# Optimization experiments

Hardware: AMD Instinct MI355X
Metric: run time of the kernel (lower is better)

Reference implementation:

```python
import jax, jax.numpy as jnp
import numpy as np

N_SUB = 60000   # nodes in current subgraph (rows of fnode/agraph/subnode)
M = 120000      # total messages (directed edges)
K = 8           # max neighbors per node/message
H = 128         # hidden_size
IN = 256        # input_size (fmess feature dim)
FD = 128        # node_fdim
DEPTH = 2       # rnn depth (sparse_forward iterations)
NUM_NODES = 65536


def setup_inputs() -> dict:
    key = jax.random.key(0)
    ks = jax.random.split(key, 12)
    s = 0.05
    def w(k, shape):
        return jax.random.normal(k, shape, jnp.float32) * s
    return {
        "fnode": jax.random.normal(ks[0], (N_SUB, FD), jnp.float32),
        "fmess": jax.random.normal(ks[1], (M, IN), jnp.float32),
        "agraph": jax.random.randint(ks[2], (N_SUB, K), 0, M, dtype=jnp.int32),
        "bgraph": jax.random.randint(ks[3], (M, K), 0, M, dtype=jnp.int32),
        "h_in": jax.random.normal(ks[4], (M, H), jnp.float32),
        "c_in": jax.random.normal(ks[5], (M, H), jnp.float32),
        "submess": jnp.arange(N_SUB, dtype=jnp.int32),
        "subnode": jnp.arange(N_SUB, dtype=jnp.int32),
        "num_nodes": NUM_NODES,
        # tree-LSTM gate weights, stored [in_dim, out_dim]
        "Wi": w(ks[6], (IN + H, H)), "bi": jnp.zeros((H,), jnp.float32),
        "Wo": w(ks[7], (IN + H, H)), "bo": jnp.zeros((H,), jnp.float32),
        "Wf": w(ks[8], (IN + H, H)), "bf": jnp.zeros((H,), jnp.float32),
        "Wu": w(ks[9], (IN + H, H)), "bu": jnp.zeros((H,), jnp.float32),
        # node readout W_o: Linear(node_fdim + hidden -> hidden) + ReLU (+ Dropout = eval no-op)
        "Wn": w(ks[10], (FD + H, H)), "bn": jnp.zeros((H,), jnp.float32),
    }


def _lstm_cell(x, h_nei, c_nei, Wi, bi, Wo, bo, Wf, bf, Wu, bu):
    # x: [S, IN]; h_nei, c_nei: [S, K, H]  (hgraph-style child-sum tree LSTM)
    h_sum = h_nei.sum(axis=1)                         # [S, H]
    z = jnp.concatenate([x, h_sum], axis=-1)          # [S, IN+H]
    i = jax.nn.sigmoid(z @ Wi + bi)
    o = jax.nn.sigmoid(z @ Wo + bo)
    u = jnp.tanh(z @ Wu + bu)
    # per-neighbor forget gate: sigmoid(cat([x_expand, h_nei]) @ Wf + bf),
    # split the matmul so we never materialize the [S, K, IN+H] concat
    d_in = x.shape[1]
    fx = x @ Wf[:d_in] + bf                           # [S, H]
    f = jax.nn.sigmoid(fx[:, None, :] + h_nei @ Wf[d_in:])  # [S, K, H]
    c = i * u + (f * c_nei).sum(axis=1)
    h = o * jnp.tanh(c)
    return h, c


def reference(fnode, fmess, agraph, bgraph, h_in, c_in, submess, subnode, num_nodes,
              Wi, bi, Wo, bo, Wf, bf, Wu, bu, Wn, bn):
    # LSTM.sparse_forward: zero state at submess rows, then iteratively update them
    mask = jnp.ones((h_in.shape[0],), h_in.dtype).at[submess].set(0.0)
    h = h_in * mask[:, None]
    c = c_in * mask[:, None]
    x_sub = fmess[submess]       # [S, IN]
    bg_sub = bgraph[submess]     # [S, K] message-neighbor ids
    for _ in range(DEPTH):
        h_nei = h[bg_sub]        # [S, K, H] gather
        c_nei = c[bg_sub]
        sub_h, sub_c = _lstm_cell(x_sub, h_nei, c_nei, Wi, bi, Wo, bo, Wf, bf, Wu, bu)
        h = h.at[submess].set(sub_h)   # index_scatter
        c = c.at[submess].set(sub_c)
    # node update: gather incoming messages, sum, Linear + ReLU (dropout inactive at eval)
    nei_message = h[agraph].sum(axis=1)                      # [N_SUB, H]
    node_hiddens = jnp.concatenate([fnode, nei_message], axis=-1)
    node_hiddens = jax.nn.relu(node_hiddens @ Wn + bn)       # [N_SUB, H]
    node_buf = jnp.zeros((num_nodes, node_hiddens.shape[1]), node_hiddens.dtype)
    node_buf = node_buf.at[subnode].set(node_hiddens)        # index_scatter into full buffer
    return node_buf, h, c
```

## Files before the change

### kernel.cpp

```cpp
#include <hip/hip_runtime.h>
#include <cstdint>
#include <cstddef>

#define Hc   128
#define INc  256
#define Kc   8
#define HP   136
#define HSP  136
#define EPH  136
#define ZP2  264
#define XOP  520

typedef unsigned short ushortT;
typedef __attribute__((ext_vector_type(8))) short bf16x8;
typedef __attribute__((ext_vector_type(4))) float f32x4;
typedef __attribute__((ext_vector_type(4))) unsigned short us4;
typedef __attribute__((ext_vector_type(8))) unsigned short us8;

__device__ __forceinline__ float fsig(float x) {
  return __builtin_amdgcn_rcpf(1.f + __expf(-x));
}
__device__ __forceinline__ float ftanh(float x) {
  float e = __expf(2.f * fminf(x, 15.f));
  return (e - 1.f) * __builtin_amdgcn_rcpf(e + 1.f);
}
__device__ __forceinline__ ushortT f2bf(float f) {
  unsigned u = __builtin_bit_cast(unsigned, f);
  unsigned r = (u + 0x7fffu + ((u >> 16) & 1u)) >> 16;
  return (ushortT)r;
}
__device__ __forceinline__ us4 f2bf4(float4 v) {
  us4 o; o[0] = f2bf(v.x); o[1] = f2bf(v.y); o[2] = f2bf(v.z); o[3] = f2bf(v.w);
  return o;
}
__device__ __forceinline__ us8 f2bf8(float4 a, float4 b) {
  us8 o;
  o[0] = f2bf(a.x); o[1] = f2bf(a.y); o[2] = f2bf(a.z); o[3] = f2bf(a.w);
  o[4] = f2bf(b.x); o[5] = f2bf(b.y); o[6] = f2bf(b.z); o[7] = f2bf(b.w);
  return o;
}
__device__ __forceinline__ float bf2f(ushortT u) {
  return __builtin_bit_cast(float, (unsigned)u << 16);
}

#define GATE_FRAGS (4*8*12*64)
#define WN_FRAGS   (8*8*64)

__global__ void marks_init(int* __restrict__ mark, int M, int* __restrict__ nmark, int NN) {
  int i = blockIdx.x * blockDim.x + threadIdx.x;
  if (i < M) mark[i] = -1;
  if (i < NN) nmark[i] = -1;
}

__global__ void set_repack(const int* __restrict__ submess, const int* __restrict__ subnode,
                           int S, int* __restrict__ mark, int* __restrict__ nmark,
                           const float* __restrict__ Wi, const float* __restrict__ Wo,
                           const float* __restrict__ Wu, const float* __restrict__ Wf,
                           const float* __restrict__ Wn, ushortT* __restrict__ pack, int SB) {
  if ((int)blockIdx.x < SB) {
    int i = blockIdx.x * 256 + threadIdx.x;
    if (i < S) { mark[submess[i]] = i; nmark[subnode[i]] = i; }
    return;
  }
  int idx = (blockIdx.x - SB) * 256 + threadIdx.x;
  if (idx < GATE_FRAGS) {
    int lane = idx & 63;
    int kt = (idx >> 6) % 12;
    int gc = idx / (64 * 12);
    int c = gc & 7, g = gc >> 3;
    const float* W = (g == 0) ? Wi : (g == 1) ? Wo : (g == 2) ? Wu : Wf;
    int k0 = kt * 32 + (lane >> 4) * 8;
    int col = c * 16 + (lane & 15);
    ushortT* dst = pack + (size_t)idx * 8;
    #pragma unroll
    for (int j = 0; j < 8; ++j) dst[j] = f2bf(W[(size_t)(k0 + j) * Hc + col]);
  } else if (idx < GATE_FRAGS + WN_FRAGS) {
    int i2 = idx - GATE_FRAGS;
    int lane = i2 & 63;
    int kt = (i2 >> 6) & 7;
    int c = i2 >> 9;
    int k0 = kt * 32 + (lane >> 4) * 8;
    int col = c * 16 + (lane & 15);
    ushortT* dst = pack + (size_t)GATE_FRAGS * 8 + (size_t)i2 * 8;
    #pragma unroll
    for (int j = 0; j < 8; ++j) dst[j] = f2bf(Wn[(size_t)(k0 + j) * Hc + col]);
  }
}

__device__ __forceinline__ const bf16x8* wh_frag(const ushortT* pack, int g, int cw, int kf, int lane) {
  return (const bf16x8*)&pack[(size_t)(((g * 8 + cw) * 12 + (8 + kf)) * 64 + lane) * 8];
}

__global__ __launch_bounds__(256) void xg_stage_hf(
    const float* __restrict__ fmess, const int* __restrict__ submess,
    const ushortT* __restrict__ pack,
    const float* __restrict__ bi, const float* __restrict__ bo,
    const float* __restrict__ bu, const float* __restrict__ bfb,
    ushortT* __restrict__ Xg,
    const float* __restrict__ h_in, const float* __restrict__ c_in,
    const int* __restrict__ mark,
    float* __restrict__ h_out, float* __restrict__ c_out,
    ushortT* __restrict__ H16x, ushortT* __restrict__ C16x, ushortT* __restrict__ Hf16x,
    int M, int S, int XB)
{
  __shared__ __align__(16) unsigned char pool[16 * XOP * 2];
  __shared__ int aux[16];
  const int t = threadIdx.x;
  const int w = t >> 6, lane = t & 63, lg = lane >> 4, cl = lane & 15;

  if ((int)blockIdx.x < XB) {
    ushortT* xs = (ushortT*)pool;
    ushortT* xo = (ushortT*)pool;
    const int row0 = blockIdx.x * 16;
    if (t < 16) aux[t] = (row0 + t < S) ? submess[row0 + t] : -1;
    __syncthreads();
    {
      int r = t >> 4, cp = t & 15;
      int ms = aux[r];
      const float4* xr = (ms >= 0) ? (const float4*)(fmess + (size_t)ms * INc) : nullptr;
      #pragma unroll
      for (int q = 0; q < 4; ++q) {
        int slot = cp + q * 16;
        float4 v;
        if (xr) v = xr[slot]; else { v.x = v.y = v.z = v.w = 0.f; }
        *(us4*)&xs[r * ZP2 + slot * 4] = f2bf4(v);
      }
    }
    __syncthreads();

    f32x4 acc[8];
    #pragma unroll
    for (int i = 0; i < 8; ++i) acc[i] = (f32x4){0.f, 0.f, 0.f, 0.f};
    const ushortT* zr = &xs[cl * ZP2 + lg * 8];
    #pragma unroll
    for (int kt = 0; kt < 8; ++kt) {
      bf16x8 a = *(const bf16x8*)&zr[kt * 32];
      #pragma unroll
      for (int c = 0; c < 8; ++c) {
        bf16x8 b = *(const bf16x8*)&pack[(size_t)(((w * 8 + c) * 12 + kt) * 64 + lane) * 8];
        acc[c] = __builtin_amdgcn_mfma_f32_16x16x32_bf16(a, b, acc[c], 0, 0, 0);
      }
    }
    __syncthreads();
    const float* bias = (w == 0) ? bi : (w == 1) ? bo : (w == 2) ? bu : bfb;
    #pragma unroll
    for (int c = 0; c < 8; ++c) {
      int col = c * 16 + cl;
      float bv = bias[col];
      #pragma unroll
      for (int reg = 0; reg < 4; ++reg)
        xo[(lg * 4 + reg) * XOP + w * 128 + col] = f2bf(acc[c][reg] + bv);
    }
    __syncthreads();
    {
      int r = t >> 4, cc = t & 15;
      int s = row0 + r;
      if (s < S) {
        const ushortT* src = &xo[r * XOP + cc * 32];
        ushortT* dst = &Xg[(size_t)s * 512 + cc * 32];
        *(us8*)&dst[0]  = *(const us8*)&src[0];
        *(us8*)&dst[8]  = *(const us8*)&src[8];
        *(us8*)&dst[16] = *(const us8*)&src[16];
        *(us8*)&dst[24] = *(const us8*)&src[24];
      }
    }
    return;
  }

  ushortT* zh = (ushortT*)pool;
  int* mk = aux;
  const int row0 = (blockIdx.x - XB) * 16;

  if (blockIdx.x == XB && t < 48) {
    int arr = t >> 4, cp = t & 15;
    ushortT* dst = (arr == 0) ? H16x : (arr == 1) ? C16x : Hf16x;
    us8 z;
    #pragma unroll
    for (int e = 0; e < 8; ++e) z[e] = 0;
    *(us8*)&dst[(size_t)(M + S) * Hc + cp * 8] = z;
  }
  if (t < 16) mk[t] = (row0 + t < M) ? mark[row0 + t] : 0;
  __syncthreads();
  {
    int r = t >> 4, cp = t & 15;
    int j = row0 + r;
    us8 hz;
    #pragma unroll
    for (int e = 0; e < 8; ++e) hz[e] = 0;
    if (j < M && mk[r] < 0) {
      const float4* h4 = (const float4*)(h_in + (size_t)j * Hc);
      const float4* c4 = (const float4*)(c_in + (size_t)j * Hc);
      float4 a0 = h4[cp * 2], a1 = h4[cp * 2 + 1];
      float4 b0 = c4[cp * 2], b1 = c4[cp * 2 + 1];
      ((float4*)(h_out + (size_t)j * Hc))[cp * 2] = a0;
      ((float4*)(h_out + (size_t)j * Hc))[cp * 2 + 1] = a1;
      ((float4*)(c_out + (size_t)j * Hc))[cp * 2] = b0;
      ((float4*)(c_out + (size_t)j * Hc))[cp * 2 + 1] = b1;
      us8 h8 = f2bf8(a0, a1);
      *(us8*)&H16x[(size_t)j * Hc + cp * 8] = h8;
      *(us8*)&C16x[(size_t)j * Hc + cp * 8] = f2bf8(b0, b1);
      hz = h8;
    }
    *(us8*)&zh[r * HP + cp * 8] = hz;
  }
  __syncthreads();

  f32x4 acc0 = (f32x4){0.f,0.f,0.f,0.f}, acc1 = acc0;
  const ushortT* zr = &zh[cl * HP + lg * 8];
  #pragma unroll
  for (int kf = 0; kf < 4; ++kf) {
    bf16x8 a = *(const bf16x8*)&zr[kf * 32];
    acc0 = __builtin_amdgcn_mfma_f32_16x16x32_bf16(a, *wh_frag(pack, 3, w*2+0, kf, lane), acc0, 0, 0, 0);
    acc1 = __builtin_amdgcn_mfma_f32_16x16x32_bf16(a, *wh_frag(pack, 3, w*2+1, kf, lane), acc1, 0, 0, 0);
  }
  __syncthreads();
  #pragma unroll
  for (int half = 0; half < 2; ++half) {
    int col = (w * 2 + half) * 16 + cl;
    f32x4 a_ = half ? acc1 : acc0;
    #pragma unroll
    for (int reg = 0; reg < 4; ++reg)
      zh[(lg * 4 + reg) * HP + col] = f2bf(a_[reg]);
  }
  __syncthreads();
  {
    int r = t >> 4, cp = t & 15;
    if (row0 + r < M && mk[r] < 0)
      *(us8*)&Hf16x[(size_t)(row0 + r) * Hc + cp * 8] = *(const us8*)&zh[r * HP + cp * 8];
  }
}

template<int MODE>
__global__ __launch_bounds__(256) void lstm8(
    const int* __restrict__ submess, const int* __restrict__ bgraph,
    const int* __restrict__ mark,
    ushortT* H16x, ushortT* C16x, ushortT* Hf16x,
    const ushortT* __restrict__ Xg, const ushortT* __restrict__ pack,
    ushortT* hsumNS, ushortT* cpartNS,
    float* __restrict__ dstH, float* __restrict__ dstC, int S, int M)
{
  __shared__ __align__(16) ushortT zs[16 * HSP];
  __shared__ __align__(16) ushortT pih[16 * EPH];
  __shared__ __align__(16) ushortT poh[16 * EPH];
  __shared__ __align__(16) ushortT puh[16 * EPH];
  __shared__ int nbj[16][Kc];
  __shared__ int msrow[16];

  const int t = threadIdx.x;
  const int row0 = blockIdx.x * 16;
  const int DUMMY = M + S;

  if (t < 128) {
    int r = t >> 3, k = t & 7;
    int s = row0 + r;
    int ms = (s < S) ? submess[s] : -1;
    if (k == 0) msrow[r] = ms;
    int j = DUMMY;
    if (ms >= 0) {
      int jj = bgraph[(size_t)ms * Kc + k];
      int m = mark[jj];
      j = (MODE == 0) ? (m >= 0 ? DUMMY : jj) : (m >= 0 ? M + m : DUMMY);
    }
    nbj[r][k] = j;
  }
  __syncthreads();

  {
    int r = t >> 4, cp = t & 15;
    int spos = row0 + r;
    float sum[8] = {0.f,0.f,0.f,0.f,0.f,0.f,0.f,0.f};
    if (MODE == 1 && spos < S) {
      us8 hs = *(const us8*)&hsumNS[(size_t)spos * Hc + cp * 8];
      #pragma unroll
      for (int e = 0; e < 8; ++e) sum[e] = bf2f(hs[e]);
    }
    #pragma unroll
    for (int k = 0; k < Kc; ++k) {
      int j = nbj[r][k];
      us8 v = *(const us8*)&H16x[(size_t)j * Hc + cp * 8];
      #pragma unroll
      for (int e = 0; e < 8; ++e) sum[e] += bf2f(v[e]);
    }
    us8 o8;
    #pragma unroll
    for (int e = 0; e < 8; ++e) o8[e] = f2bf(sum[e]);
    *(us8*)&zs[r * HSP + cp * 8] = o8;
    if (MODE == 0 && spos < S)
      *(us8*)&hsumNS[(size_t)spos * Hc + cp * 8] = o8;
  }
  __syncthreads();

  const int w = t >> 6, lane = t & 63, lg = lane >> 4, cl = lane & 15;

  f32x4 acc[6];
  #pragma unroll
  for (int i = 0; i < 6; ++i) acc[i] = (f32x4){0.f, 0.f, 0.f, 0.f};
  const ushortT* zrow = &zs[cl * HSP + lg * 8];
  #pragma unroll
  for (int kf = 0; kf < 4; ++kf) {
    bf16x8 a = *(const bf16x8*)&zrow[kf * 32];
    #pragma unroll
    for (int g = 0; g < 3; ++g)
      #pragma unroll
      for (int half = 0; half < 2; ++half)
        acc[g * 2 + half] = __builtin_amdgcn_mfma_f32_16x16x32_bf16(
            a, *wh_frag(pack, g, w * 2 + half, kf, lane), acc[g * 2 + half], 0, 0, 0);
  }

  #pragma unroll
  for (int half = 0; half < 2; ++half) {
    int col = (w * 2 + half) * 16 + cl;
    #pragma unroll
    for (int reg = 0; reg < 4; ++reg) {
      int row = lg * 4 + reg;
      pih[row * EPH + col] = f2bf(acc[0 + half][reg]);
      poh[row * EPH + col] = f2bf(acc[2 + half][reg]);
      puh[row * EPH + col] = f2bf(acc[4 + half][reg]);
    }
  }
  __syncthreads();

  {
    int r = t >> 4, cc = t & 15;
    int ms = msrow[r];
    int spos = row0 + r;
    const ushortT* xgr = Xg + (size_t)spos * 512 + cc * 8;
    us8 xi8 = *(const us8*)&xgr[0];
    us8 xo8 = *(const us8*)&xgr[128];
    us8 xu8 = *(const us8*)&xgr[256];
    us8 xf8 = *(const us8*)&xgr[384];
    us8 pi8 = *(const us8*)&pih[r * EPH + cc * 8];
    us8 po8 = *(const us8*)&poh[r * EPH + cc * 8];
    us8 pu8 = *(const us8*)&puh[r * EPH + cc * 8];
    float fx[8], ovv[8], iu[8], cn[8];
    #pragma unroll
    for (int e = 0; e < 8; ++e) {
      float iv = fsig(bf2f(xi8[e]) + bf2f(pi8[e]));
      float uv = ftanh(bf2f(xu8[e]) + bf2f(pu8[e]));
      ovv[e] = fsig(bf2f(xo8[e]) + bf2f(po8[e]));
      fx[e] = bf2f(xf8[e]);
      iu[e] = iv * uv;
      cn[e] = 0.f;
    }
    #pragma unroll
    for (int k = 0; k < Kc; ++k) {
      int j = nbj[r][k];
      us8 hf8 = *(const us8*)&Hf16x[(size_t)j * Hc + cc * 8];
      us8 cn8 = *(const us8*)&C16x[(size_t)j * Hc + cc * 8];
      #pragma unroll
      for (int e = 0; e < 8; ++e)
        cn[e] = fmaf(fsig(fx[e] + bf2f(hf8[e])), bf2f(cn8[e]), cn[e]);
    }
    float cacc[8];
    if (MODE == 1 && spos < S) {
      us8 cp8 = *(const us8*)&cpartNS[(size_t)spos * Hc + cc * 8];
      #pragma unroll
      for (int e = 0; e < 8; ++e) cacc[e] = iu[e] + cn[e] + bf2f(cp8[e]);
    } else {
      #pragma unroll
      for (int e = 0; e < 8; ++e) cacc[e] = iu[e] + cn[e];
    }
    float hv[8];
    #pragma unroll
    for (int e = 0; e < 8; ++e) hv[e] = ovv[e] * ftanh(cacc[e]);

    if (MODE == 0) {
      us8 h8, c8, cn16;
      #pragma unroll
      for (int e = 0; e < 8; ++e) {
        h8[e] = (spos < S) ? f2bf(hv[e]) : (ushortT)0;
        c8[e] = f2bf(cacc[e]);
        cn16[e] = f2bf(cn[e]);
      }
      if (spos < S) {
        *(us8*)&H16x[(size_t)(M + spos) * Hc + cc * 8] = h8;
        *(us8*)&C16x[(size_t)(M + spos) * Hc + cc * 8] = c8;
        *(us8*)&cpartNS[(size_t)spos * Hc + cc * 8] = cn16;
      }
      *(us8*)&zs[r * HSP + cc * 8] = h8;
    } else {
      if (ms >= 0) {
        float* dh = dstH + (size_t)ms * Hc + cc * 8;
        float* dc = dstC + (size_t)ms * Hc + cc * 8;
        *(float4*)&dh[0] = *(float4*)&hv[0];
        *(float4*)&dh[4] = *(float4*)&hv[4];
        *(float4*)&dc[0] = *(float4*)&cacc[0];
        *(float4*)&dc[4] = *(float4*)&cacc[4];
      }
    }
  }

  if (MODE == 0) {
    __syncthreads();
    f32x4 a0 = (f32x4){0.f,0.f,0.f,0.f}, a1 = a0;
    const ushortT* zr2 = &zs[cl * HSP + lg * 8];
    #pragma unroll
    for (int kf = 0; kf < 4; ++kf) {
      bf16x8 a = *(const bf16x8*)&zr2[kf * 32];
      a0 = __builtin_amdgcn_mfma_f32_16x16x32_bf16(a, *wh_frag(pack, 3, w*2+0, kf, lane), a0, 0, 0, 0);
      a1 = __builtin_amdgcn_mfma_f32_16x16x32_bf16(a, *wh_frag(pack, 3, w*2+1, kf, lane), a1, 0, 0, 0);
    }
    #pragma unroll
    for (int half = 0; half < 2; ++half) {
      int col = (w * 2 + half) * 16 + cl;
      f32x4 a_ = half ? a1 : a0;
      #pragma unroll
      for (int reg = 0; reg < 4; ++reg)
        pih[(lg * 4 + reg) * EPH + col] = f2bf(a_[reg]);
    }
    __syncthreads();
    {
      int r = t >> 4, cp = t & 15;
      int sp = row0 + r;
      if (sp < S)
        *(us8*)&Hf16x[(size_t)(M + sp) * Hc + cp * 8] = *(const us8*)&pih[r * EPH + cp * 8];
    }
  }
}

__global__ __launch_bounds__(256) void readout_zero(
    const float* __restrict__ fnode, const int* __restrict__ agraph,
    const int* __restrict__ subnode, const float* __restrict__ h_out,
    const ushortT* __restrict__ H16x, const int* __restrict__ mark,
    const int* __restrict__ nmark,
    const ushortT* __restrict__ packWn, const float* __restrict__ bn,
    float* __restrict__ node_buf, int Nsub, int num_nodes, int NB, int ZB)
{
  __shared__ __align__(16) ushortT z2[16 * ZP2];
  __shared__ int orow[16];
  __shared__ int jn[16][Kc];

  const int t = threadIdx.x;

  if ((int)blockIdx.x >= NB) {
    long total = (long)num_nodes * 16;
    float4 z; z.x = z.y = z.z = z.w = 0.f;
    for (long idx = (long)(blockIdx.x - NB) * 256 + t; idx < total; idx += (long)ZB * 256) {
      long v = idx >> 4;
      int cp = (int)(idx & 15);
      if (nmark[v] < 0) {
        ((float4*)(node_buf + (size_t)v * Hc))[cp * 2] = z;
        ((float4*)(node_buf + (size_t)v * Hc))[cp * 2 + 1] = z;
      }
    }
    return;
  }

  const int row0 = blockIdx.x * 16;
  if (t < 16) orow[t] = (row0 + t < Nsub) ? subnode[row0 + t] : -1;
  if (t >= 64 && t < 64 + 128) {
    int i = t - 64, r = i >> 3, k = i & 7;
    int v = row0 + r;
    int j = 0;
    if (v < Nsub) {
      j = agraph[(size_t)v * Kc + k];
      if (mark[j] >= 0) j = ~j;
    }
    jn[r][k] = j;
  }
  {
    int r = t >> 4, cp = t & 15;
    int v = row0 + r;
    const float4* fr = (v < Nsub) ? (const float4*)(fnode + (size_t)v * Hc) : nullptr;
    float4 v0, v1; v0.x = v0.y = v0.z = v0.w = 0.f; v1 = v0;
    if (fr) { v0 = fr[cp]; v1 = fr[cp + 16]; }
    *(us4*)&z2[r * ZP2 + cp * 4] = f2bf4(v0);
    *(us4*)&z2[r * ZP2 + 64 + cp * 4] = f2bf4(v1);
  }
  __syncthreads();
  {
    int r = t >> 4, cp = t & 15;
    float sum[8] = {0.f,0.f,0.f,0.f,0.f,0.f,0.f,0.f};
    #pragma unroll
    for (int k = 0; k < Kc; ++k) {
      int je = jn[r][k];
      if (je < 0) {
        int j = ~je;
        float4 p0 = ((const float4*)(h_out + (size_t)j * Hc))[cp * 2];
        float4 p1 = ((const float4*)(h_out + (size_t)j * Hc))[cp * 2 + 1];
        sum[0] += p0.x; sum[1] += p0.y; sum[2] += p0.z; sum[3] += p0.w;
        sum[4] += p1.x; sum[5] += p1.y; sum[6] += p1.z; sum[7] += p1.w;
      } else {
        us8 v = *(const us8*)&H16x[(size_t)je * Hc + cp * 8];
        #pragma unroll
        for (int e = 0; e < 8; ++e) sum[e] += bf2f(v[e]);
      }
    }
    us8 o8;
    #pragma unroll
    for (int e = 0; e < 8; ++e) o8[e] = f2bf(sum[e]);
    *(us8*)&z2[r * ZP2 + Hc + cp * 8] = o8;
  }
  __syncthreads();

  const int w = t >> 6, lane = t & 63;
  const int lg = lane >> 4, cl = lane & 15;

  f32x4 acc0 = (f32x4){0.f,0.f,0.f,0.f};
  f32x4 acc1 = (f32x4){0.f,0.f,0.f,0.f};
  const ushortT* zr = &z2[cl * ZP2 + lg * 8];
  #pragma unroll
  for (int kt = 0; kt < 8; ++kt) {
    bf16x8 a = *(const bf16x8*)&zr[kt * 32];
    bf16x8 b0 = *(const bf16x8*)&packWn[(size_t)(((w * 2 + 0) * 8 + kt) * 64 + lane) * 8];
    bf16x8 b1 = *(const bf16x8*)&packWn[(size_t)(((w * 2 + 1) * 8 + kt) * 64 + lane) * 8];
    acc0 = __builtin_amdgcn_mfma_f32_16x16x32_bf16(a, b0, acc0, 0, 0, 0);
    acc1 = __builtin_amdgcn_mfma_f32_16x16x32_bf16(a, b1, acc1, 0, 0, 0);
  }
  __syncthreads();
  float* zf = (float*)z2;
  #pragma unroll
  for (int half = 0; half < 2; ++half) {
    int col = (w * 2 + half) * 16 + cl;
    float bnv = bn[col];
    f32x4 a_ = half ? acc1 : acc0;
    #pragma unroll
    for (int reg = 0; reg < 4; ++reg)
      zf[(lg * 4 + reg) * 132 + col] = fmaxf(a_[reg] + bnv, 0.f);
  }
  __syncthreads();
  {
    int r = t >> 4, cc = t & 15;
    int o = orow[r];
    if (o >= 0) {
      float* dst = node_buf + (size_t)o * Hc + cc * 8;
      *(float4*)&dst[0] = *(const float4*)&zf[r * 132 + cc * 8];
      *(float4*)&dst[4] = *(const float4*)&zf[r * 132 + cc * 8 + 4];
    }
  }
}

extern "C" void kernel_launch(void* const* d_in, const int* in_sizes, int n_in,
                              void* d_out, int out_size, void* d_ws, size_t ws_size,
                              hipStream_t stream) {
  const float* fnode   = (const float*)d_in[0];
  const float* fmess   = (const float*)d_in[1];
  const int*   agraph  = (const int*)d_in[2];
  const int*   bgraph  = (const int*)d_in[3];
  const float* h_in    = (const float*)d_in[4];
  const float* c_in    = (const float*)d_in[5];
  const int*   submess = (const int*)d_in[6];
  const int*   subnode = (const int*)d_in[7];
  const float* Wi = (const float*)d_in[9];
  const float* bi = (const float*)d_in[10];
  const float* Wo = (const float*)d_in[11];
  const float* bo = (const float*)d_in[12];
  const float* Wf = (const float*)d_in[13];
  const float* bf_ = (const float*)d_in[14];
  const float* Wu = (const float*)d_in[15];
  const float* bu = (const float*)d_in[16];
  const float* Wn = (const float*)d_in[17];
  const float* bn = (const float*)d_in[18];

  const int S    = in_sizes[6];
  const int Nsub = in_sizes[2] / Kc;
  const int M    = in_sizes[4] / Hc;
  const int num_nodes = out_size / Hc - 2 * M;

  float* node_buf = (float*)d_out;
  float* h_out = node_buf + (size_t)num_nodes * Hc;
  float* c_out = h_out + (size_t)M * Hc;

  const int lblocks = (S + 15) / 16;

  int* mark = (int*)d_ws;
  size_t off = (((size_t)M * sizeof(int)) + 255) & ~(size_t)255;
  int* nmark = (int*)((char*)d_ws + off);
  off += (((size_t)num_nodes * sizeof(int)) + 255) & ~(size_t)255;
  ushortT* pack = (ushortT*)((char*)d_ws + off);
  off += (((size_t)(GATE_FRAGS + WN_FRAGS) * 8 * sizeof(ushortT)) + 255) & ~(size_t)255;
  size_t shadow_bytes = (((size_t)(M + S + 1) * Hc * sizeof(ushortT)) + 255) & ~(size_t)255;
  ushortT* Hf16x = (ushortT*)((char*)d_ws + off); off += shadow_bytes;
  ushortT* C16x  = (ushortT*)((char*)d_ws + off); off += shadow_bytes;
  ushortT* H16x  = (ushortT*)((char*)d_ws + off); off += shadow_bytes;
  ushortT* Xg    = (ushortT*)((char*)d_ws + off);
  ushortT* packWn = pack + (size_t)GATE_FRAGS * 8;
  ushortT* cpartNS = (ushortT*)node_buf;
  ushortT* hsumNS  = cpartNS + (size_t)S * Hc;

  int initN = (M > num_nodes) ? M : num_nodes;
  hipLaunchKernelGGL(marks_init, dim3((initN + 255) / 256), dim3(256), 0, stream,
                     mark, M, nmark, num_nodes);
  {
    int SB = (S + 255) / 256;
    int RB = (GATE_FRAGS + WN_FRAGS + 255) / 256;
    hipLaunchKernelGGL(set_repack, dim3(SB + RB), dim3(256), 0, stream,
                       submess, subnode, S, mark, nmark, Wi, Wo, Wu, Wf, Wn, pack, SB);
  }
  {
    int XB = lblocks;
    int SB2 = (M + 15) / 16;
    hipLaunchKernelGGL(xg_stage_hf, dim3(XB + SB2), dim3(256), 0, stream,
                       fmess, submess, pack, bi, bo, bu, bf_, Xg,
                       h_in, c_in, mark, h_out, c_out, H16x, C16x, Hf16x,
                       M, S, XB);
  }
  hipLaunchKernelGGL(lstm8<0>, dim3(lblocks), dim3(256), 0, stream,
      submess, bgraph, mark, H16x, C16x, Hf16x, Xg, pack,
      hsumNS, cpartNS, h_out, c_out, S, M);
  hipLaunchKernelGGL(lstm8<1>, dim3(lblocks), dim3(256), 0, stream,
      submess, bgraph, mark, H16x, C16x, Hf16x, Xg, pack,
      hsumNS, cpartNS, h_out, c_out, S, M);
  {
    int NB = (Nsub + 15) / 16;
    int ZB = 512;
    hipLaunchKernelGGL(readout_zero, dim3(NB + ZB), dim3(256), 0, stream,
        fnode, agraph, subnode, h_out, H16x, mark, nmark, packWn, bn,
        node_buf, Nsub, num_nodes, NB, ZB);
  }
}
```

Baseline: 278.6 us.

## Interleave H/C/Hf bf16 shadows into one row array and double rows per Xg block

Merges the three separate bf16 shadow arrays (H, C, forget-gate H projection) into one interleaved array with a 384-element row stride, so a neighbor gather of c and hf for the same message hits adjacent memory in one row. Separately, the Xg precompute blocks now handle 32 rows instead of 16, reusing each loaded weight fragment for two MFMA row tiles. The first targets scattered gather traffic across three buffers; the second halves weight fragment reloads in the input projection at the cost of more accumulator registers and fewer blocks. The H-only gathers now stride over larger rows, which may reduce cache-line density for those reads.

```diff
diff --git a/kernel.cpp b/kernel.cpp
--- a/kernel.cpp
+++ b/kernel.cpp
@@ -10,6 +10,7 @@
 #define EPH  136
 #define ZP2  264
 #define XOP  520
+#define HCS  384
 
 typedef unsigned short ushortT;
 typedef __attribute__((ext_vector_type(8))) short bf16x8;
@@ -100,22 +101,21 @@
     const float* __restrict__ h_in, const float* __restrict__ c_in,
     const int* __restrict__ mark,
     float* __restrict__ h_out, float* __restrict__ c_out,
-    ushortT* __restrict__ H16x, ushortT* __restrict__ C16x, ushortT* __restrict__ Hf16x,
+    ushortT* __restrict__ HCF,
     int M, int S, int XB)
 {
-  __shared__ __align__(16) unsigned char pool[16 * XOP * 2];
-  __shared__ int aux[16];
+  __shared__ __align__(16) ushortT xs[32 * ZP2];
+  __shared__ int aux[32];
   const int t = threadIdx.x;
   const int w = t >> 6, lane = t & 63, lg = lane >> 4, cl = lane & 15;
 
   if ((int)blockIdx.x < XB) {
-    ushortT* xs = (ushortT*)pool;
-    ushortT* xo = (ushortT*)pool;
-    const int row0 = blockIdx.x * 16;
-    if (t < 16) aux[t] = (row0 + t < S) ? submess[row0 + t] : -1;
+    const int row0 = blockIdx.x * 32;
+    if (t < 32) aux[t] = (row0 + t < S) ? submess[row0 + t] : -1;
     __syncthreads();
-    {
-      int r = t >> 4, cp = t & 15;
+    #pragma unroll
+    for (int rr = 0; rr < 2; ++rr) {
+      int r = (t >> 4) + rr * 16, cp = t & 15;
       int ms = aux[r];
       const float4* xr = (ms >= 0) ? (const float4*)(fmess + (size_t)ms * INc) : nullptr;
       #pragma unroll
@@ -128,56 +128,66 @@
     }
     __syncthreads();
 
-    f32x4 acc[8];
-    #pragma unroll
-    for (int i = 0; i < 8; ++i) acc[i] = (f32x4){0.f, 0.f, 0.f, 0.f};
-    const ushortT* zr = &xs[cl * ZP2 + lg * 8];
+    f32x4 acc0[8], acc1[8];
+    #pragma unroll
+    for (int i = 0; i < 8; ++i) {
+      acc0[i] = (f32x4){0.f, 0.f, 0.f, 0.f};
+      acc1[i] = (f32x4){0.f, 0.f, 0.f, 0.f};
+    }
+    const ushortT* zrA = &xs[cl * ZP2 + lg * 8];
+    const ushortT* zrB = &xs[(16 + cl) * ZP2 + lg * 8];
     #pragma unroll
     for (int kt = 0; kt < 8; ++kt) {
-      bf16x8 a = *(const bf16x8*)&zr[kt * 32];
+      bf16x8 a0 = *(const bf16x8*)&zrA[kt * 32];
+      bf16x8 a1 = *(const bf16x8*)&zrB[kt * 32];
       #pragma unroll
       for (int c = 0; c < 8; ++c) {
         bf16x8 b = *(const bf16x8*)&pack[(size_t)(((w * 8 + c) * 12 + kt) * 64 + lane) * 8];
-        acc[c] = __builtin_amdgcn_mfma_f32_16x16x32_bf16(a, b, acc[c], 0, 0, 0);
+        acc0[c] = __builtin_amdgcn_mfma_f32_16x16x32_bf16(a0, b, acc0[c], 0, 0, 0);
+        acc1[c] = __builtin_amdgcn_mfma_f32_16x16x32_bf16(a1, b, acc1[c], 0, 0, 0);
       }
     }
     __syncthreads();
     const float* bias = (w == 0) ? bi : (w == 1) ? bo : (w == 2) ? bu : bfb;
     #pragma unroll
-    for (int c = 0; c < 8; ++c) {
-      int col = c * 16 + cl;
-      float bv = bias[col];
-      #pragma unroll
-      for (int reg = 0; reg < 4; ++reg)
-        xo[(lg * 4 + reg) * XOP + w * 128 + col] = f2bf(acc[c][reg] + bv);
-    }
-    __syncthreads();
-    {
-      int r = t >> 4, cc = t & 15;
-      int s = row0 + r;
-      if (s < S) {
-        const ushortT* src = &xo[r * XOP + cc * 32];
-        ushortT* dst = &Xg[(size_t)s * 512 + cc * 32];
-        *(us8*)&dst[0]  = *(const us8*)&src[0];
-        *(us8*)&dst[8]  = *(const us8*)&src[8];
-        *(us8*)&dst[16] = *(const us8*)&src[16];
-        *(us8*)&dst[24] = *(const us8*)&src[24];
-      }
+    for (int mt = 0; mt < 2; ++mt) {
+      #pragma unroll
+      for (int c = 0; c < 8; ++c) {
+        int col = c * 16 + cl;
+        float bv = bias[col];
+        #pragma unroll
+        for (int reg = 0; reg < 4; ++reg) {
+          float v = (mt ? acc1[c][reg] : acc0[c][reg]) + bv;
+          xs[(lg * 4 + reg) * XOP + w * 128 + col] = f2bf(v);
+        }
+      }
+      __syncthreads();
+      {
+        int r = t >> 4, cc = t & 15;
+        int s = row0 + mt * 16 + r;
+        if (s < S) {
+          const ushortT* src = &xs[r * XOP + cc * 32];
+          ushortT* dst = &Xg[(size_t)s * 512 + cc * 32];
+          *(us8*)&dst[0]  = *(const us8*)&src[0];
+          *(us8*)&dst[8]  = *(const us8*)&src[8];
+          *(us8*)&dst[16] = *(const us8*)&src[16];
+          *(us8*)&dst[24] = *(const us8*)&src[24];
+        }
+      }
+      __syncthreads();
     }
     return;
   }
 
-  ushortT* zh = (ushortT*)pool;
+  ushortT* zh = xs;
   int* mk = aux;
   const int row0 = (blockIdx.x - XB) * 16;
 
   if (blockIdx.x == XB && t < 48) {
-    int arr = t >> 4, cp = t & 15;
-    ushortT* dst = (arr == 0) ? H16x : (arr == 1) ? C16x : Hf16x;
     us8 z;
     #pragma unroll
     for (int e = 0; e < 8; ++e) z[e] = 0;
-    *(us8*)&dst[(size_t)(M + S) * Hc + cp * 8] = z;
+    *(us8*)&HCF[(size_t)(M + S) * HCS + t * 8] = z;
   }
   if (t < 16) mk[t] = (row0 + t < M) ? mark[row0 + t] : 0;
   __syncthreads();
@@ -197,8 +207,8 @@
       ((float4*)(c_out + (size_t)j * Hc))[cp * 2] = b0;
       ((float4*)(c_out + (size_t)j * Hc))[cp * 2 + 1] = b1;
       us8 h8 = f2bf8(a0, a1);
-      *(us8*)&H16x[(size_t)j * Hc + cp * 8] = h8;
-      *(us8*)&C16x[(size_t)j * Hc + cp * 8] = f2bf8(b0, b1);
+      *(us8*)&HCF[(size_t)j * HCS + cp * 8] = h8;
+      *(us8*)&HCF[(size_t)j * HCS + 128 + cp * 8] = f2bf8(b0, b1);
       hz = h8;
     }
     *(us8*)&zh[r * HP + cp * 8] = hz;
@@ -226,7 +236,7 @@
   {
     int r = t >> 4, cp = t & 15;
     if (row0 + r < M && mk[r] < 0)
-      *(us8*)&Hf16x[(size_t)(row0 + r) * Hc + cp * 8] = *(const us8*)&zh[r * HP + cp * 8];
+      *(us8*)&HCF[(size_t)(row0 + r) * HCS + 256 + cp * 8] = *(const us8*)&zh[r * HP + cp * 8];
   }
 }
 
@@ -234,7 +244,7 @@
 __global__ __launch_bounds__(256) void lstm8(
     const int* __restrict__ submess, const int* __restrict__ bgraph,
     const int* __restrict__ mark,
-    ushortT* H16x, ushortT* C16x, ushortT* Hf16x,
+    ushortT* HCF,
     const ushortT* __restrict__ Xg, const ushortT* __restrict__ pack,
     ushortT* hsumNS, ushortT* cpartNS,
     float* __restrict__ dstH, float* __restrict__ dstC, int S, int M)
@@ -277,7 +287,7 @@
     #pragma unroll
     for (int k = 0; k < Kc; ++k) {
       int j = nbj[r][k];
-      us8 v = *(const us8*)&H16x[(size_t)j * Hc + cp * 8];
+      us8 v = *(const us8*)&HCF[(size_t)j * HCS + cp * 8];
       #pragma unroll
       for (int e = 0; e < 8; ++e) sum[e] += bf2f(v[e]);
     }
@@ -345,8 +355,8 @@
     #pragma unroll
     for (int k = 0; k < Kc; ++k) {
       int j = nbj[r][k];
-      us8 hf8 = *(const us8*)&Hf16x[(size_t)j * Hc + cc * 8];
-      us8 cn8 = *(const us8*)&C16x[(size_t)j * Hc + cc * 8];
+      us8 hf8 = *(const us8*)&HCF[(size_t)j * HCS + 256 + cc * 8];
+      us8 cn8 = *(const us8*)&HCF[(size_t)j * HCS + 128 + cc * 8];
       #pragma unroll
       for (int e = 0; e < 8; ++e)
         cn[e] = fmaf(fsig(fx[e] + bf2f(hf8[e])), bf2f(cn8[e]), cn[e]);
@@ -373,8 +383,8 @@
         cn16[e] = f2bf(cn[e]);
       }
       if (spos < S) {
-        *(us8*)&H16x[(size_t)(M + spos) * Hc + cc * 8] = h8;
-        *(us8*)&C16x[(size_t)(M + spos) * Hc + cc * 8] = c8;
+        *(us8*)&HCF[(size_t)(M + spos) * HCS + cc * 8] = h8;
+        *(us8*)&HCF[(size_t)(M + spos) * HCS + 128 + cc * 8] = c8;
         *(us8*)&cpartNS[(size_t)spos * Hc + cc * 8] = cn16;
       }
       *(us8*)&zs[r * HSP + cc * 8] = h8;
@@ -413,7 +423,7 @@
       int r = t >> 4, cp = t & 15;
       int sp = row0 + r;
       if (sp < S)
-        *(us8*)&Hf16x[(size_t)(M + sp) * Hc + cp * 8] = *(const us8*)&pih[r * EPH + cp * 8];
+        *(us8*)&HCF[(size_t)(M + sp) * HCS + 256 + cp * 8] = *(const us8*)&pih[r * EPH + cp * 8];
     }
   }
 }
@@ -421,7 +431,7 @@
 __global__ __launch_bounds__(256) void readout_zero(
     const float* __restrict__ fnode, const int* __restrict__ agraph,
     const int* __restrict__ subnode, const float* __restrict__ h_out,
-    const ushortT* __restrict__ H16x, const int* __restrict__ mark,
+    const ushortT* __restrict__ HCF, const int* __restrict__ mark,
     const int* __restrict__ nmark,
     const ushortT* __restrict__ packWn, const float* __restrict__ bn,
     float* __restrict__ node_buf, int Nsub, int num_nodes, int NB, int ZB)
@@ -481,7 +491,7 @@
         sum[0] += p0.x; sum[1] += p0.y; sum[2] += p0.z; sum[3] += p0.w;
         sum[4] += p1.x; sum[5] += p1.y; sum[6] += p1.z; sum[7] += p1.w;
       } else {
-        us8 v = *(const us8*)&H16x[(size_t)je * Hc + cp * 8];
+        us8 v = *(const us8*)&HCF[(size_t)je * HCS + cp * 8];
         #pragma unroll
         for (int e = 0; e < 8; ++e) sum[e] += bf2f(v[e]);
       }
@@ -569,11 +579,9 @@
   off += (((size_t)num_nodes * sizeof(int)) + 255) & ~(size_t)255;
   ushortT* pack = (ushortT*)((char*)d_ws + off);
   off += (((size_t)(GATE_FRAGS + WN_FRAGS) * 8 * sizeof(ushortT)) + 255) & ~(size_t)255;
-  size_t shadow_bytes = (((size_t)(M + S + 1) * Hc * sizeof(ushortT)) + 255) & ~(size_t)255;
-  ushortT* Hf16x = (ushortT*)((char*)d_ws + off); off += shadow_bytes;
-  ushortT* C16x  = (ushortT*)((char*)d_ws + off); off += shadow_bytes;
-  ushortT* H16x  = (ushortT*)((char*)d_ws + off); off += shadow_bytes;
-  ushortT* Xg    = (ushortT*)((char*)d_ws + off);
+  ushortT* HCF = (ushortT*)((char*)d_ws + off);
+  off += (((size_t)(M + S + 1) * HCS * sizeof(ushortT)) + 255) & ~(size_t)255;
+  ushortT* Xg = (ushortT*)((char*)d_ws + off);
   ushortT* packWn = pack + (size_t)GATE_FRAGS * 8;
   ushortT* cpartNS = (ushortT*)node_buf;
   ushortT* hsumNS  = cpartNS + (size_t)S * Hc;
@@ -588,24 +596,24 @@
                        submess, subnode, S, mark, nmark, Wi, Wo, Wu, Wf, Wn, pack, SB);
   }
   {
-    int XB = lblocks;
+    int XB = (S + 31) / 32;
     int SB2 = (M + 15) / 16;
     hipLaunchKernelGGL(xg_stage_hf, dim3(XB + SB2), dim3(256), 0, stream,
                        fmess, submess, pack, bi, bo, bu, bf_, Xg,
-                       h_in, c_in, mark, h_out, c_out, H16x, C16x, Hf16x,
+                       h_in, c_in, mark, h_out, c_out, HCF,
                        M, S, XB);
   }
   hipLaunchKernelGGL(lstm8<0>, dim3(lblocks), dim3(256), 0, stream,
-      submess, bgraph, mark, H16x, C16x, Hf16x, Xg, pack,
+      submess, bgraph, mark, HCF, Xg, pack,
       hsumNS, cpartNS, h_out, c_out, S, M);
   hipLaunchKernelGGL(lstm8<1>, dim3(lblocks), dim3(256), 0, stream,
-      submess, bgraph, mark, H16x, C16x, Hf16x, Xg, pack,
+      submess, bgraph, mark, HCF, Xg, pack,
       hsumNS, cpartNS, h_out, c_out, S, M);
   {
     int NB = (Nsub + 15) / 16;
     int ZB = 512;
     hipLaunchKernelGGL(readout_zero, dim3(NB + ZB), dim3(256), 0, stream,
-        fnode, agraph, subnode, h_out, H16x, mark, nmark, packWn, bn,
+        fnode, agraph, subnode, h_out, HCF, mark, nmark, packWn, bn,
         node_buf, Nsub, num_nodes, NB, ZB);
   }
 }
```

Result: no change. 276.6 us (-0.7%).
